# Optimization experiments

Hardware: AMD Instinct MI355X
Metric: run time of the kernel (lower is better)

The kernel has to match this reference:

```python
import jax, jax.numpy as jnp
import numpy as np

jax.config.update("jax_enable_x64", True)  # torch path computes in float64

MAX_BIT = 31
ACT_BIT = 8


def setup_inputs() -> dict:
    key = jax.random.key(0)
    k1, k2, k3, k4 = jax.random.split(key, 4)
    B, S, D = 8, 4096, 768
    x = jax.random.normal(k1, (B, S, D), dtype=jnp.float32)
    identity = jax.random.normal(k2, (B, S, D), dtype=jnp.float32)
    pre_act_scaling_factor = jax.random.uniform(k3, (D,), jnp.float32, 1e-3, 1e-2)
    identity_scaling_factor = jax.random.uniform(k4, (D,), jnp.float32, 1e-3, 1e-2)
    return {
        "x": x,
        "pre_act_scaling_factor": pre_act_scaling_factor,
        "identity": identity,
        "identity_scaling_factor": identity_scaling_factor,
    }


def _batch_frexp(v):
    # v > 0 (ratios of positive scales). frexp: v = m * 2**e with m in [0.5, 1).
    m, e = jnp.frexp(v.astype(jnp.float64))
    # Decimal ROUND_HALF_UP of m * 2**31 (m positive -> floor(x + 0.5))
    m_int = jnp.floor(m * (2.0 ** MAX_BIT) + 0.5)
    e_out = jnp.asarray(MAX_BIT, jnp.float64) - e.astype(jnp.float64)
    return m_int, e_out


def reference(x, pre_act_scaling_factor, identity, identity_scaling_factor):
    n = 2 ** (ACT_BIT - 1) - 1  # 127

    # ----- running-stat range tracking (min_val == max_val == 0 initially) -----
    x_act = x + identity
    min_val = x_act.min()
    max_val = x_act.max()
    eps = jnp.finfo(jnp.float32).eps
    z_scale = jnp.maximum(jnp.maximum(-min_val, max_val) / float(n), eps)  # scalar

    # ----- fixedpoint_mul (symmetric, bit_num=8) -----
    pre = pre_act_scaling_factor.reshape(1, 1, -1)   # [1,1,D]
    ids = identity_scaling_factor.reshape(1, 1, -1)  # [1,1,D]

    z_int = jnp.round(x / pre)  # banker's rounding, matches torch.round
    m, e = _batch_frexp(pre.astype(jnp.float64) / z_scale.astype(jnp.float64))
    output = jnp.round(z_int.astype(jnp.float64) * m / (2.0 ** e))

    wx_int = jnp.round(identity / ids)
    m1, e1 = _batch_frexp(ids.astype(jnp.float64) / z_scale.astype(jnp.float64))
    output1 = jnp.round(wx_int.astype(jnp.float64) * m1 / (2.0 ** e1))

    quant_int = jnp.clip((output + output1).astype(jnp.float32), -n - 1, n)

    out = quant_int * z_scale.astype(jnp.float32)
    return out, z_scale.reshape(1)
```

## Files before the change

kernel.cpp:

```cpp
#include <hip/hip_runtime.h>
#include <math.h>

static constexpr int kD = 768;
static constexpr int kRows = 8 * 4096;
static constexpr long long kN = (long long)kRows * kD;
static constexpr int kVec = (int)(kN / 4);
static constexpr int kColGroups = kD / 4;

static constexpr int kAmaxBlocks  = 2048;
static constexpr int kQuantBlocks = 1536;

typedef float nf4 __attribute__((ext_vector_type(4)));

__global__ __launch_bounds__(256, 4) void amax_kernel(
    const float4* __restrict__ x, const float4* __restrict__ idn,
    unsigned int* __restrict__ amax_bits)
{
    const int GS = kAmaxBlocks * 256;
    const int tid = blockIdx.x * blockDim.x + threadIdx.x;
    float4 m4 = make_float4(0.f, 0.f, 0.f, 0.f);

    #pragma unroll 1
    for (int outer = 0; outer < 2; ++outer) {
        const int base = tid + outer * 6 * GS;
        float4 a[6], b[6];
        #pragma unroll
        for (int j = 0; j < 6; ++j) a[j] = x[base + j * GS];
        #pragma unroll
        for (int j = 0; j < 6; ++j) b[j] = idn[base + j * GS];
        #pragma unroll
        for (int j = 0; j < 6; ++j) {
            m4.x = fmaxf(m4.x, fabsf(a[j].x + b[j].x));
            m4.y = fmaxf(m4.y, fabsf(a[j].y + b[j].y));
            m4.z = fmaxf(m4.z, fabsf(a[j].z + b[j].z));
            m4.w = fmaxf(m4.w, fabsf(a[j].w + b[j].w));
        }
    }
    float m = fmaxf(fmaxf(m4.x, m4.y), fmaxf(m4.z, m4.w));
    #pragma unroll
    for (int off = 32; off > 0; off >>= 1)
        m = fmaxf(m, __shfl_down(m, off, 64));
    if ((threadIdx.x & 63) == 0)
        atomicMax(amax_bits, __float_as_uint(m));
}

__device__ inline double quant_factor(double r) {
    int e;
    double mm = frexp(r, &e);
    double m_int = floor(mm * 2147483648.0 + 0.5);
    return ldexp(m_int, e - 31);
}

__global__ __launch_bounds__(256) void factor_kernel(
    const float* __restrict__ pre, const float* __restrict__ ids,
    const unsigned int* __restrict__ amax_bits,
    double* __restrict__ fp, double* __restrict__ fi,
    float* __restrict__ out_scale)
{
    const float amax = __uint_as_float(*amax_bits);
    const float z_scale = fmaxf(amax / 127.0f, 1.1920928955078125e-07f);
    const int d = blockIdx.x * blockDim.x + threadIdx.x;
    if (d == 0) *out_scale = z_scale;
    if (d < kD) {
        const double zs = (double)z_scale;
        fp[d] = quant_factor((double)pre[d] / zs);
        fi[d] = quant_factor((double)ids[d] / zs);
    }
}

__device__ inline float requant_elem(float xx, float ii, float p, float s,
                                     double fp, double fi, float z_scale) {
    float z_int = rintf(xx / p);
    float w_int = rintf(ii / s);
    double o  = rint((double)z_int * fp);
    double o1 = rint((double)w_int * fi);
    float q = (float)(o + o1);
    q = fminf(fmaxf(q, -128.0f), 127.0f);
    return q * z_scale;
}

__global__ __launch_bounds__(256, 4) void quant_kernel(
    const float4* __restrict__ x, const float4* __restrict__ idn,
    const float4* __restrict__ pre, const float4* __restrict__ ids,
    const unsigned int* __restrict__ amax_bits,
    const double* __restrict__ fp_tab, const double* __restrict__ fi_tab,
    nf4* __restrict__ out)
{
    const float amax = __uint_as_float(*amax_bits);
    const float z_scale = fmaxf(amax / 127.0f, 1.1920928955078125e-07f);

    const int GS = kQuantBlocks * 256;
    const int tid = blockIdx.x * blockDim.x + threadIdx.x;
    const int cg = tid % kColGroups;

    const float4 pf = pre[cg];
    const float4 sf = ids[cg];
    double fp[4], fi[4];
    #pragma unroll
    for (int j = 0; j < 4; ++j) { fp[j] = fp_tab[4*cg + j]; fi[j] = fi_tab[4*cg + j]; }

    #pragma unroll 1
    for (int outer = 0; outer < 4; ++outer) {
        const int base = tid + outer * 4 * GS;
        float4 xa[4], ia[4];
        #pragma unroll
        for (int j = 0; j < 4; ++j) xa[j] = x[base + j * GS];
        #pragma unroll
        for (int j = 0; j < 4; ++j) ia[j] = idn[base + j * GS];
        #pragma unroll
        for (int j = 0; j < 4; ++j) {
            nf4 ov;
            ov.x = requant_elem(xa[j].x, ia[j].x, pf.x, sf.x, fp[0], fi[0], z_scale);
            ov.y = requant_elem(xa[j].y, ia[j].y, pf.y, sf.y, fp[1], fi[1], z_scale);
            ov.z = requant_elem(xa[j].z, ia[j].z, pf.z, sf.z, fp[2], fi[2], z_scale);
            ov.w = requant_elem(xa[j].w, ia[j].w, pf.w, sf.w, fp[3], fi[3], z_scale);
            __builtin_nontemporal_store(ov, &out[base + j * GS]);
        }
    }
}

extern "C" void kernel_launch(void* const* d_in, const int* in_sizes, int n_in,
                              void* d_out, int out_size, void* d_ws, size_t ws_size,
                              hipStream_t stream) {
    const float* x   = (const float*)d_in[0];
    const float* pre = (const float*)d_in[1];
    const float* idn = (const float*)d_in[2];
    const float* ids = (const float*)d_in[3];
    float* out = (float*)d_out;

    unsigned int* amax_bits = (unsigned int*)d_ws;
    double* fp_tab = (double*)((char*)d_ws + 64);
    double* fi_tab = fp_tab + kD;
    (void)hipMemsetAsync(d_ws, 0, sizeof(unsigned int), stream);

    amax_kernel<<<kAmaxBlocks, 256, 0, stream>>>(
        (const float4*)x, (const float4*)idn, amax_bits);
    factor_kernel<<<3, 256, 0, stream>>>(pre, ids, amax_bits, fp_tab, fi_tab,
                                         out + kN);
    quant_kernel<<<kQuantBlocks, 256, 0, stream>>>(
        (const float4*)x, (const float4*)idn,
        (const float4*)pre, (const float4*)ids,
        amax_bits, fp_tab, fi_tab, (nf4*)out);
}
```

Baseline: 323.9 us.

## Remap both kernels to contiguous 16-row tiles with XCD-swizzled block order

Both the amax and quant kernels switch from grid-stride float4 indexing to 192-thread blocks. Each block owns 16 contiguous rows, and each thread owns one fixed column group. Block IDs are swizzled across the 8 XCDs so neighbouring tiles go to different dies. sched_barrier calls are added to keep all loads grouped ahead of the compute. The intent is more local, contiguous memory access per block, better L2/MALL locality across XCDs, and simpler per-thread scale indexing, at the cost of smaller blocks and fixed scheduling.

```diff
diff --git a/kernel.cpp b/kernel.cpp
--- a/kernel.cpp
+++ b/kernel.cpp
@@ -2,39 +2,44 @@
 #include <math.h>
 
 static constexpr int kD = 768;
-static constexpr int kRows = 8 * 4096;
+static constexpr int kRows = 32768;
 static constexpr long long kN = (long long)kRows * kD;
-static constexpr int kVec = (int)(kN / 4);
-static constexpr int kColGroups = kD / 4;
-
-static constexpr int kAmaxBlocks  = 2048;
-static constexpr int kQuantBlocks = 1536;
+static constexpr int kColGroups = 192;
+static constexpr int kBlocks = 2048;
+static constexpr int kRowsPerBlock = 16;
 
 typedef float nf4 __attribute__((ext_vector_type(4)));
 
-__global__ __launch_bounds__(256, 4) void amax_kernel(
+__device__ __forceinline__ int swizzled_block() {
+    return (int)((blockIdx.x & 7) * (kBlocks >> 3) + (blockIdx.x >> 3));
+}
+
+__global__ __launch_bounds__(192, 4) void amax_kernel(
     const float4* __restrict__ x, const float4* __restrict__ idn,
     unsigned int* __restrict__ amax_bits)
 {
-    const int GS = kAmaxBlocks * 256;
-    const int tid = blockIdx.x * blockDim.x + threadIdx.x;
+    const int b = swizzled_block();
+    const int t = threadIdx.x;
+    const int base = b * (kRowsPerBlock * kColGroups) + t;
+
     float4 m4 = make_float4(0.f, 0.f, 0.f, 0.f);
-
     #pragma unroll 1
-    for (int outer = 0; outer < 2; ++outer) {
-        const int base = tid + outer * 6 * GS;
-        float4 a[6], b[6];
+    for (int outer = 0; outer < 4; ++outer) {
+        const int rb = base + outer * 4 * kColGroups;
+        float4 a[4], c[4];
         #pragma unroll
-        for (int j = 0; j < 6; ++j) a[j] = x[base + j * GS];
+        for (int j = 0; j < 4; ++j) a[j] = x[rb + j * kColGroups];
         #pragma unroll
-        for (int j = 0; j < 6; ++j) b[j] = idn[base + j * GS];
+        for (int j = 0; j < 4; ++j) c[j] = idn[rb + j * kColGroups];
+        __builtin_amdgcn_sched_barrier(0);
         #pragma unroll
-        for (int j = 0; j < 6; ++j) {
-            m4.x = fmaxf(m4.x, fabsf(a[j].x + b[j].x));
-            m4.y = fmaxf(m4.y, fabsf(a[j].y + b[j].y));
-            m4.z = fmaxf(m4.z, fabsf(a[j].z + b[j].z));
-            m4.w = fmaxf(m4.w, fabsf(a[j].w + b[j].w));
+        for (int j = 0; j < 4; ++j) {
+            m4.x = fmaxf(m4.x, fabsf(a[j].x + c[j].x));
+            m4.y = fmaxf(m4.y, fabsf(a[j].y + c[j].y));
+            m4.z = fmaxf(m4.z, fabsf(a[j].z + c[j].z));
+            m4.w = fmaxf(m4.w, fabsf(a[j].w + c[j].w));
         }
+        __builtin_amdgcn_sched_barrier(0);
     }
     float m = fmaxf(fmaxf(m4.x, m4.y), fmaxf(m4.z, m4.w));
     #pragma unroll
@@ -79,7 +84,7 @@
     return q * z_scale;
 }
 
-__global__ __launch_bounds__(256, 4) void quant_kernel(
+__global__ __launch_bounds__(192, 4) void quant_kernel(
     const float4* __restrict__ x, const float4* __restrict__ idn,
     const float4* __restrict__ pre, const float4* __restrict__ ids,
     const unsigned int* __restrict__ amax_bits,
@@ -89,24 +94,25 @@
     const float amax = __uint_as_float(*amax_bits);
     const float z_scale = fmaxf(amax / 127.0f, 1.1920928955078125e-07f);
 
-    const int GS = kQuantBlocks * 256;
-    const int tid = blockIdx.x * blockDim.x + threadIdx.x;
-    const int cg = tid % kColGroups;
+    const int b = swizzled_block();
+    const int t = threadIdx.x;
+    const int base = b * (kRowsPerBlock * kColGroups) + t;
 
-    const float4 pf = pre[cg];
-    const float4 sf = ids[cg];
+    const float4 pf = pre[t];
+    const float4 sf = ids[t];
     double fp[4], fi[4];
     #pragma unroll
-    for (int j = 0; j < 4; ++j) { fp[j] = fp_tab[4*cg + j]; fi[j] = fi_tab[4*cg + j]; }
+    for (int j = 0; j < 4; ++j) { fp[j] = fp_tab[4*t + j]; fi[j] = fi_tab[4*t + j]; }
 
     #pragma unroll 1
     for (int outer = 0; outer < 4; ++outer) {
-        const int base = tid + outer * 4 * GS;
+        const int rb = base + outer * 4 * kColGroups;
         float4 xa[4], ia[4];
         #pragma unroll
-        for (int j = 0; j < 4; ++j) xa[j] = x[base + j * GS];
+        for (int j = 0; j < 4; ++j) xa[j] = x[rb + j * kColGroups];
         #pragma unroll
-        for (int j = 0; j < 4; ++j) ia[j] = idn[base + j * GS];
+        for (int j = 0; j < 4; ++j) ia[j] = idn[rb + j * kColGroups];
+        __builtin_amdgcn_sched_barrier(0);
         #pragma unroll
         for (int j = 0; j < 4; ++j) {
             nf4 ov;
@@ -114,8 +120,9 @@
             ov.y = requant_elem(xa[j].y, ia[j].y, pf.y, sf.y, fp[1], fi[1], z_scale);
             ov.z = requant_elem(xa[j].z, ia[j].z, pf.z, sf.z, fp[2], fi[2], z_scale);
             ov.w = requant_elem(xa[j].w, ia[j].w, pf.w, sf.w, fp[3], fi[3], z_scale);
-            __builtin_nontemporal_store(ov, &out[base + j * GS]);
+            __builtin_nontemporal_store(ov, &out[rb + j * kColGroups]);
         }
+        __builtin_amdgcn_sched_barrier(0);
     }
 }
 
@@ -133,11 +140,11 @@
     double* fi_tab = fp_tab + kD;
     (void)hipMemsetAsync(d_ws, 0, sizeof(unsigned int), stream);
 
-    amax_kernel<<<kAmaxBlocks, 256, 0, stream>>>(
+    amax_kernel<<<kBlocks, 192, 0, stream>>>(
         (const float4*)x, (const float4*)idn, amax_bits);
     factor_kernel<<<3, 256, 0, stream>>>(pre, ids, amax_bits, fp_tab, fi_tab,
                                          out + kN);
-    quant_kernel<<<kQuantBlocks, 256, 0, stream>>>(
+    quant_kernel<<<kBlocks, 192, 0, stream>>>(
         (const float4*)x, (const float4*)idn,
         (const float4*)pre, (const float4*)ids,
         amax_bits, fp_tab, fi_tab, (nf4*)out);
```

Result: faster. 309.9 us (-4.3%).
